# Kernel optimization log

Measured on AMD Instinct MI355X. Metric: run time of the kernel, lower is better.

## Reference

```python
import jax, jax.numpy as jnp
import numpy as np

N = 100000   # nodes
E = 1600000  # edges
IN = 41      # in_channels (21 atom + 20 residue)
ED = 8       # edge_dim
H = 64       # hidden_dim
L = 3        # num_layers
G = 256      # graphs in batch
ATOM = 21
EPS = 1e-5   # GraphNorm eps


def setup_inputs() -> dict:
    key = jax.random.key(0)
    ks = jax.random.split(key, 32)
    s = 0.1
    x = jax.random.normal(ks[0], (N, IN), jnp.float32)
    # make even-index nodes 'ligand' atoms (zero residue part) so both MLP branches fire
    lig = (jnp.arange(N) % 2) == 0
    x = x.at[:, ATOM:].set(jnp.where(lig[:, None], 0.0, x[:, ATOM:]))
    edge_index = jax.random.randint(ks[1], (2, E), 0, N)
    edge_attr = jax.random.normal(ks[2], (E, ED), jnp.float32)
    batch = jnp.sort(jax.random.randint(ks[3], (N,), 0, G))
    p = {
        "lig_W1": s * jax.random.normal(ks[4], (IN, H), jnp.float32),
        "lig_b1": jnp.zeros((H,), jnp.float32),
        "lig_W2": s * jax.random.normal(ks[5], (H, H), jnp.float32),
        "lig_b2": jnp.zeros((H,), jnp.float32),
        "prot_W1": s * jax.random.normal(ks[6], (IN, H), jnp.float32),
        "prot_b1": jnp.zeros((H,), jnp.float32),
        "prot_W2": s * jax.random.normal(ks[7], (H, H), jnp.float32),
        "prot_b2": jnp.zeros((H,), jnp.float32),
        # per-layer stacked params for the 3 GINEConv + GraphNorm blocks
        "conv_We": s * jax.random.normal(ks[8], (L, ED, H), jnp.float32),
        "conv_be": jnp.zeros((L, H), jnp.float32),
        "conv_W1": s * jax.random.normal(ks[9], (L, H, H), jnp.float32),
        "conv_b1": jnp.zeros((L, H), jnp.float32),
        "conv_W2": s * jax.random.normal(ks[10], (L, H, H), jnp.float32),
        "conv_b2": jnp.zeros((L, H), jnp.float32),
        "norm_w": jnp.ones((L, H), jnp.float32),
        "norm_b": jnp.zeros((L, H), jnp.float32),
        "norm_a": jnp.ones((L, H), jnp.float32),  # mean_scale alpha
        "out_W1": s * jax.random.normal(ks[11], (H, H), jnp.float32),
        "out_b1": jnp.zeros((H,), jnp.float32),
        "out_W2": s * jax.random.normal(ks[12], (H, 1), jnp.float32),
        "out_b2": jnp.zeros((1,), jnp.float32),
    }
    return dict(x=x, edge_index=edge_index, edge_attr=edge_attr, batch=batch, **p)


def reference(x, edge_index, edge_attr, batch,
              lig_W1, lig_b1, lig_W2, lig_b2,
              prot_W1, prot_b1, prot_W2, prot_b2,
              conv_We, conv_be, conv_W1, conv_b1, conv_W2, conv_b2,
              norm_w, norm_b, norm_a,
              out_W1, out_b1, out_W2, out_b2):
    # --- input encoder: ligand vs protein branch by residue-part mask ---
    res_mask = jnp.sum(jnp.abs(x[:, ATOM:]), axis=1) > 1e-6
    h_lig = jax.nn.relu(jax.nn.relu(x @ lig_W1 + lig_b1) @ lig_W2 + lig_b2)
    h_prot = jax.nn.relu(jax.nn.relu(x @ prot_W1 + prot_b1) @ prot_W2 + prot_b2)
    h = jnp.where(res_mask[:, None], h_prot, h_lig)  # [N, H]

    src, dst = edge_index[0], edge_index[1]
    counts = jnp.maximum(jax.ops.segment_sum(jnp.ones((N,), h.dtype), batch,
                                             num_segments=G), 1.0)[:, None]  # [G,1]

    for l in range(L):
        # GINEConv (eps=0): nn(h_i + sum_j relu(h_j + lin(e_ij)))
        e = edge_attr @ conv_We[l] + conv_be[l]           # [E, H]
        msg = jax.nn.relu(h[src] + e)                     # [E, H]
        aggr = jax.ops.segment_sum(msg, dst, num_segments=N)
        z = h + aggr
        h = jax.nn.relu(z @ conv_W1[l] + conv_b1[l]) @ conv_W2[l] + conv_b2[l]
        # GraphNorm: (h - alpha*mean_g) / sqrt(var_g + eps) * w + b
        mean = jax.ops.segment_sum(h, batch, num_segments=G) / counts  # [G, H]
        out = h - norm_a[l] * mean[batch]
        var = jax.ops.segment_sum(out * out, batch, num_segments=G) / counts
        h = norm_w[l] * (out / jnp.sqrt(var + EPS)[batch]) + norm_b[l]
        h = jax.nn.relu(h)

    # global_add_pool + readout (dropout = identity at eval)
    g = jax.ops.segment_sum(h, batch, num_segments=G)  # [G, H]
    out = jax.nn.relu(g @ out_W1 + out_b1) @ out_W2 + out_b2  # [G, 1]
    return out.reshape(-1)
```

## Files before the change

### kernel.cpp

```cpp
#include <hip/hip_runtime.h>

#define NN 100000
#define NE 1600000
#define IN_CH 41
#define EDIM 8
#define H 64
#define GNUM 256
#define ATOM 21
#define EPSV 1e-5f
#define EPW 16
#define NTILE (NN / 16)

#define BSH 9
#define NBK 196
#define DPB 512
#define VPT 8
#define EPB (256 * VPT)
#define NBLK_E ((NE + EPB - 1) / EPB)

typedef unsigned short u16;
typedef unsigned int u32;
typedef unsigned long long u64;
typedef __attribute__((ext_vector_type(8))) short short8;
typedef __attribute__((ext_vector_type(4))) float floatx4;

__device__ __forceinline__ u16 f2bf(float f) {
    u32 u = __float_as_uint(f);
    u32 r = (u + 0x7FFFu + ((u >> 16) & 1u)) >> 16;
    return (u16)r;
}
__device__ __forceinline__ float bf2f(u16 u) {
    return __uint_as_float(((u32)u) << 16);
}
__device__ __forceinline__ floatx4 mfma16(short8 a, short8 b, floatx4 c) {
    return __builtin_amdgcn_mfma_f32_16x16x32_bf16(a, b, c, 0, 0, 0);
}
__device__ __forceinline__ short8 pack_bf8(float4 a, float4 b) {
    short8 s;
    s[0] = (short)f2bf(a.x); s[1] = (short)f2bf(a.y);
    s[2] = (short)f2bf(a.z); s[3] = (short)f2bf(a.w);
    s[4] = (short)f2bf(b.x); s[5] = (short)f2bf(b.y);
    s[6] = (short)f2bf(b.z); s[7] = (short)f2bf(b.w);
    return s;
}

__global__ __launch_bounds__(256) void partition_kernel(
    const float* __restrict__ x, int* __restrict__ ctr,
    int* __restrict__ lig_list, int* __restrict__ prot_list)
{
    const int n = blockIdx.x * 256 + threadIdx.x;
    const int lane = threadIdx.x & 63;
    float m = 0.0f;
    if (n < NN) {
        const float* xr = x + (size_t)n * IN_CH + ATOM;
#pragma unroll
        for (int d = 0; d < IN_CH - ATOM; ++d) m += fabsf(xr[d]);
    }
    const bool valid = n < NN;
    const bool prot = valid && (m > 1e-6f);
    const bool lig = valid && !prot;

    const u64 bl = __ballot(lig);
    const u64 bp = __ballot(prot);
    const u64 below_m = (lane == 63) ? (~0ull >> 1) : ((1ull << lane) - 1ull);
    int base_l = 0, base_p = 0;
    if (lane == 0) {
        if (bl) base_l = atomicAdd(&ctr[0], (int)__popcll(bl));
        if (bp) base_p = atomicAdd(&ctr[1], (int)__popcll(bp));
    }
    base_l = __shfl(base_l, 0, 64);
    base_p = __shfl(base_p, 0, 64);
    if (lig)  lig_list [base_l + (int)__popcll(bl & below_m)] = n;
    if (prot) prot_list[base_p + (int)__popcll(bp & below_m)] = n;
}

__global__ __launch_bounds__(256) void xb_kernel(
    const float* __restrict__ x, u16* __restrict__ xb)
{
    const int id = blockIdx.x * 256 + threadIdx.x;
    if (id >= NN * H) return;
    const int n = id >> 6, d = id & 63;
    xb[id] = (d < IN_CH) ? f2bf(x[(size_t)n * IN_CH + d]) : (u16)0;
}

__global__ __launch_bounds__(256) void prep_w_kernel(
    const float* __restrict__ ligW1, const float* __restrict__ ligW2,
    const float* __restrict__ protW1, const float* __restrict__ protW2,
    const float* __restrict__ convW1, const float* __restrict__ convW2,
    u16* __restrict__ wf)
{
    const int id = blockIdx.x * 256 + threadIdx.x;
    if (id >= 10 * 4096) return;
    const int j = id & 7, l = (id >> 3) & 63, t = (id >> 9) & 3;
    const int c = (id >> 11) & 1, mat = id >> 12;
    const int k = c * 32 + ((l >> 4) * 8) + j;
    const int n = t * 16 + (l & 15);
    const float* src; int K = 64;
    if (mat == 0)      { src = ligW1;  K = IN_CH; }
    else if (mat == 1) { src = ligW2; }
    else if (mat == 2) { src = protW1; K = IN_CH; }
    else if (mat == 3) { src = protW2; }
    else {
        const int layer = (mat - 4) >> 1;
        src = (((mat - 4) & 1) ? convW2 : convW1) + (size_t)layer * H * H;
    }
    wf[id] = (k < K) ? f2bf(src[(size_t)k * H + n]) : (u16)0;
}

__global__ __launch_bounds__(256) void enc_mfma_kernel(
    const int* __restrict__ list, const int* __restrict__ countPtr,
    const u16* __restrict__ xb,
    const u16* __restrict__ w1f, const u16* __restrict__ w2f,
    const float* __restrict__ bia1, const float* __restrict__ bia2,
    float* __restrict__ h, u16* __restrict__ h16)
{
    __shared__ __align__(16) u16 hid[4][16 * 72];
    const int wv = threadIdx.x >> 6;
    const int lane = threadIdx.x & 63;
    const int tile = blockIdx.x * 4 + wv;
    const int count = *countPtr;
    if (tile * 16 >= count) return;
    const int quad = lane >> 4;
    const int mi = lane & 15;
    int idx = tile * 16 + mi;
    if (idx >= count) idx = count - 1;
    const int nid = list[idx];

    const short8 a0 = *(const short8*)(xb + (size_t)nid * H + quad * 8);
    const short8 a1 = *(const short8*)(xb + (size_t)nid * H + 32 + quad * 8);

    floatx4 acc[4];
#pragma unroll
    for (int t = 0; t < 4; ++t) acc[t] = (floatx4){0.f, 0.f, 0.f, 0.f};
#pragma unroll
    for (int t = 0; t < 4; ++t) {
        const short8 b0 = *(const short8*)(w1f + ((size_t)(0 * 4 + t) * 64 + lane) * 8);
        const short8 b1 = *(const short8*)(w1f + ((size_t)(1 * 4 + t) * 64 + lane) * 8);
        acc[t] = mfma16(a0, b0, acc[t]);
        acc[t] = mfma16(a1, b1, acc[t]);
    }

    u16* myh = hid[wv];
#pragma unroll
    for (int t = 0; t < 4; ++t) {
        const float bv = bia1[t * 16 + mi];
#pragma unroll
        for (int r = 0; r < 4; ++r) {
            const float v = fmaxf(acc[t][r] + bv, 0.0f);
            myh[(quad * 4 + r) * 72 + t * 16 + mi] = f2bf(v);
        }
    }
    asm volatile("s_waitcnt lgkmcnt(0)" ::: "memory");

    const short8 c0 = *(const short8*)(myh + mi * 72 + quad * 8);
    const short8 c1 = *(const short8*)(myh + mi * 72 + 32 + quad * 8);

    floatx4 acc2[4];
#pragma unroll
    for (int t = 0; t < 4; ++t) acc2[t] = (floatx4){0.f, 0.f, 0.f, 0.f};
#pragma unroll
    for (int t = 0; t < 4; ++t) {
        const short8 b0 = *(const short8*)(w2f + ((size_t)(0 * 4 + t) * 64 + lane) * 8);
        const short8 b1 = *(const short8*)(w2f + ((size_t)(1 * 4 + t) * 64 + lane) * 8);
        acc2[t] = mfma16(c0, b0, acc2[t]);
        acc2[t] = mfma16(c1, b1, acc2[t]);
    }

#pragma unroll
    for (int t = 0; t < 4; ++t) {
        const float bv = bia2[t * 16 + mi];
#pragma unroll
        for (int r = 0; r < 4; ++r) {
            const int row = quad * 4 + r;
            const int nr = __shfl(nid, row, 64);
            if (tile * 16 + row < count) {
                const float v = fmaxf(acc2[t][r] + bv, 0.0f);
                h[(size_t)nr * H + t * 16 + mi] = v;
                h16[(size_t)nr * H + t * 16 + mi] = f2bf(v);
            }
        }
    }
}

__global__ __launch_bounds__(256) void mlp_mfma_kernel(
    const u16* __restrict__ w1f, const u16* __restrict__ w2f,
    const float* __restrict__ bia1, const float* __restrict__ bia2,
    float* __restrict__ h)
{
    __shared__ __align__(16) u16 hid[4][16 * 72];
    const int wv = threadIdx.x >> 6;
    const int lane = threadIdx.x & 63;
    const int tile = blockIdx.x * 4 + wv;
    if (tile >= NTILE) return;
    const int quad = lane >> 4;
    const int mi = lane & 15;
    const int row = tile * 16 + mi;
    const float* zr = h + (size_t)row * H;

    const float4 f0 = *(const float4*)(zr + quad * 8);
    const float4 f1 = *(const float4*)(zr + quad * 8 + 4);
    const float4 f2 = *(const float4*)(zr + 32 + quad * 8);
    const float4 f3 = *(const float4*)(zr + 32 + quad * 8 + 4);
    const short8 a0 = pack_bf8(f0, f1);
    const short8 a1 = pack_bf8(f2, f3);

    floatx4 acc[4];
#pragma unroll
    for (int t = 0; t < 4; ++t) acc[t] = (floatx4){0.f, 0.f, 0.f, 0.f};
#pragma unroll
    for (int t = 0; t < 4; ++t) {
        const short8 b0 = *(const short8*)(w1f + ((size_t)(0 * 4 + t) * 64 + lane) * 8);
        const short8 b1 = *(const short8*)(w1f + ((size_t)(1 * 4 + t) * 64 + lane) * 8);
        acc[t] = mfma16(a0, b0, acc[t]);
        acc[t] = mfma16(a1, b1, acc[t]);
    }

    u16* myh = hid[wv];
#pragma unroll
    for (int t = 0; t < 4; ++t) {
        const float bv = bia1[t * 16 + mi];
#pragma unroll
        for (int r = 0; r < 4; ++r) {
            const float v = fmaxf(acc[t][r] + bv, 0.0f);
            myh[(quad * 4 + r) * 72 + t * 16 + mi] = f2bf(v);
        }
    }
    asm volatile("s_waitcnt lgkmcnt(0)" ::: "memory");

    const short8 c0 = *(const short8*)(myh + mi * 72 + quad * 8);
    const short8 c1 = *(const short8*)(myh + mi * 72 + 32 + quad * 8);

    floatx4 acc2[4];
#pragma unroll
    for (int t = 0; t < 4; ++t) acc2[t] = (floatx4){0.f, 0.f, 0.f, 0.f};
#pragma unroll
    for (int t = 0; t < 4; ++t) {
        const short8 b0 = *(const short8*)(w2f + ((size_t)(0 * 4 + t) * 64 + lane) * 8);
        const short8 b1 = *(const short8*)(w2f + ((size_t)(1 * 4 + t) * 64 + lane) * 8);
        acc2[t] = mfma16(c0, b0, acc2[t]);
        acc2[t] = mfma16(c1, b1, acc2[t]);
    }

#pragma unroll
    for (int t = 0; t < 4; ++t) {
        const float bv = bia2[t * 16 + mi];
#pragma unroll
        for (int r = 0; r < 4; ++r) {
            const int orow = tile * 16 + quad * 4 + r;
            h[(size_t)orow * H + t * 16 + mi] = acc2[t][r] + bv;
        }
    }
}

__global__ void bounds_kernel(const int* __restrict__ batch, int* __restrict__ start)
{
    int g = blockIdx.x * blockDim.x + threadIdx.x;
    if (g > GNUM) return;
    int lo = 0, hi = NN;
    while (lo < hi) {
        int mid = (lo + hi) >> 1;
        if (batch[mid] < g) lo = mid + 1; else hi = mid;
    }
    start[g] = lo;
}

__global__ __launch_bounds__(256) void bhist_kernel(
    const int* __restrict__ ei, int* __restrict__ gbcount)
{
    __shared__ int cnt[NBK];
    const int t = threadIdx.x;
    if (t < NBK) cnt[t] = 0;
    __syncthreads();
    const int base = blockIdx.x * EPB;
#pragma unroll
    for (int v = 0; v < VPT; ++v) {
        const int e = base + v * 256 + t;
        if (e < NE) atomicAdd(&cnt[ei[NE + e] >> BSH], 1);
    }
    __syncthreads();
    if (t < NBK && cnt[t]) atomicAdd(&gbcount[t], cnt[t]);
}

__global__ __launch_bounds__(256) void bscan_kernel(
    const int* __restrict__ gbcount, int* __restrict__ gstart, int* __restrict__ gcur)
{
    __shared__ int s[256];
    const int t = threadIdx.x;
    int v = (t < NBK) ? gbcount[t] : 0;
    s[t] = v;
    __syncthreads();
#pragma unroll
    for (int off = 1; off < 256; off <<= 1) {
        int tmp = (t >= off) ? s[t - off] : 0;
        __syncthreads();
        s[t] += tmp;
        __syncthreads();
    }
    if (t < NBK) { gstart[t] = s[t] - v; gcur[t] = s[t] - v; }
    if (t == 0) gstart[NBK] = NE;
}

__global__ __launch_bounds__(256) void p1_kernel(
    const int* __restrict__ ei, const float* __restrict__ ea,
    int* __restrict__ gcur,
    int2* __restrict__ tmp_sd, uint4* __restrict__ tmp_eab)
{
    __shared__ int cnt[NBK];
    __shared__ int cur[NBK];
    const int t = threadIdx.x;
    if (t < NBK) cnt[t] = 0;
    __syncthreads();
    const int base = blockIdx.x * EPB;
    int dstv[VPT];
#pragma unroll
    for (int v = 0; v < VPT; ++v) {
        const int e = base + v * 256 + t;
        dstv[v] = -1;
        if (e < NE) {
            dstv[v] = ei[NE + e];
            atomicAdd(&cnt[dstv[v] >> BSH], 1);
        }
    }
    __syncthreads();
    if (t < NBK) cur[t] = cnt[t] ? atomicAdd(&gcur[t], cnt[t]) : 0;
    __syncthreads();
#pragma unroll
    for (int v = 0; v < VPT; ++v) {
        const int e = base + v * 256 + t;
        if (e < NE) {
            const int b = dstv[v] >> BSH;
            const int pos = atomicAdd(&cur[b], 1);
            tmp_sd[pos] = make_int2(ei[e], dstv[v]);
            const float4* e4 = (const float4*)(ea + (size_t)e * EDIM);
            float4 a = e4[0], bb = e4[1];
            uint4 u;
            u.x = (u32)f2bf(a.x) | ((u32)f2bf(a.y) << 16);
            u.y = (u32)f2bf(a.z) | ((u32)f2bf(a.w) << 16);
            u.z = (u32)f2bf(bb.x) | ((u32)f2bf(bb.y) << 16);
            u.w = (u32)f2bf(bb.z) | ((u32)f2bf(bb.w) << 16);
            tmp_eab[pos] = u;
        }
    }
}

__global__ __launch_bounds__(1024) void sort_kernel(
    const int2* __restrict__ tmp_sd, const uint4* __restrict__ tmp_eab,
    const int* __restrict__ gstart,
    int2* __restrict__ perm2, uint4* __restrict__ eab)
{
    __shared__ int hist[DPB];
    __shared__ int cursor[DPB];
    const int b = blockIdx.x;
    const int t = threadIdx.x;
    const int s = gstart[b], e = gstart[b + 1];
    const int dbase = b << BSH;

    if (t < DPB) hist[t] = 0;
    __syncthreads();
    for (int i = s + t; i < e; i += 1024)
        atomicAdd(&hist[tmp_sd[i].y - dbase], 1);
    __syncthreads();
    if (t < DPB) cursor[t] = hist[t];
    __syncthreads();
#pragma unroll
    for (int off = 1; off < DPB; off <<= 1) {
        int v = (t < DPB && t >= off) ? cursor[t - off] : 0;
        __syncthreads();
        if (t < DPB) cursor[t] += v;
        __syncthreads();
    }
    if (t < DPB) cursor[t] = s + cursor[t] - hist[t];
    __syncthreads();
    for (int i = s + t; i < e; i += 1024) {
        const int2 sd = tmp_sd[i];
        const int pos = atomicAdd(&cursor[sd.y - dbase], 1);
        perm2[pos] = sd;
        eab[pos] = tmp_eab[i];
    }
}

__global__ __launch_bounds__(256) void aggr_kernel(
    const int2* __restrict__ perm2,
    const u32* __restrict__ eab32,
    const float* __restrict__ We, const float* __restrict__ be,
    const u16* __restrict__ h16, float* __restrict__ h)
{
    const int lane = threadIdx.x & 63;
    const int chunk = blockIdx.x * 4 + (threadIdx.x >> 6);
    const int base = chunk * EPW;

    float we_r[EDIM];
#pragma unroll
    for (int d = 0; d < EDIM; ++d) we_r[d] = We[d * H + lane];
    const float be_r = be[lane];

    const int2 pd = perm2[base + (lane & 15)];
    const u32 eu = eab32[(size_t)base * 4 + lane];

    float hv[EPW];
#pragma unroll
    for (int j = 0; j < EPW; ++j) {
        const int sj = __builtin_amdgcn_readlane(pd.x, j);
        hv[j] = bf2f(h16[(size_t)sj * H + lane]);
    }

    float acc = 0.0f;
    int cur = __builtin_amdgcn_readlane(pd.y, 0);
#pragma unroll
    for (int j = 0; j < EPW; ++j) {
        const int dj = __builtin_amdgcn_readlane(pd.y, j);
        float msg = be_r;
#pragma unroll
        for (int p = 0; p < 4; ++p) {
            const u32 w2 = __builtin_amdgcn_readlane(eu, j * 4 + p);
            msg = fmaf(__uint_as_float(w2 << 16), we_r[2 * p], msg);
            msg = fmaf(__uint_as_float(w2 & 0xffff0000u), we_r[2 * p + 1], msg);
        }
        if (dj != cur) {
            unsafeAtomicAdd(&h[(size_t)cur * H + lane], acc);
            acc = 0.0f;
            cur = dj;
        }
        acc += fmaxf(hv[j] + msg, 0.0f);
    }
    unsafeAtomicAdd(&h[(size_t)cur * H + lane], acc);
}

__global__ __launch_bounds__(1024) void graphnorm_kernel(
    float* __restrict__ h, u16* __restrict__ h16,
    const int* __restrict__ start,
    const float* __restrict__ w, const float* __restrict__ b,
    const float* __restrict__ a,
    float* __restrict__ pool, int do_pool)
{
    __shared__ float red1[16][H], red2[16][H];
    __shared__ float amean_s[H], rstd_s[H];
    const int g = blockIdx.x;
    const int lane = threadIdx.x & 63;
    const int wv = threadIdx.x >> 6;
    const int s = start[g], e = start[g + 1];

    float s1 = 0.f, s2 = 0.f;
    for (int i = s + wv; i < e; i += 16) {
        float v = h[(size_t)i * H + lane];
        s1 += v; s2 += v * v;
    }
    red1[wv][lane] = s1; red2[wv][lane] = s2;
    __syncthreads();
    if (threadIdx.x < H) {
        float t1 = 0.f, t2 = 0.f;
#pragma unroll
        for (int k = 0; k < 16; ++k) { t1 += red1[k][lane]; t2 += red2[k][lane]; }
        float cnt = fmaxf((float)(e - s), 1.0f);
        float mean = t1 / cnt;
        float alpha = a[lane];
        float var = t2 / cnt - (2.0f * alpha - alpha * alpha) * mean * mean;
        var = fmaxf(var, 0.0f);
        amean_s[lane] = alpha * mean;
        rstd_s[lane] = rsqrtf(var + EPSV);
    }
    __syncthreads();
    const float am = amean_s[lane], rstd = rstd_s[lane];
    const float ww = w[lane], bb = b[lane];
    float ps = 0.f;
    for (int i = s + wv; i < e; i += 16) {
        float v = (h[(size_t)i * H + lane] - am) * rstd * ww + bb;
        v = fmaxf(v, 0.0f);
        h[(size_t)i * H + lane] = v;
        h16[(size_t)i * H + lane] = f2bf(v);
        ps += v;
    }
    if (do_pool && e > s) unsafeAtomicAdd(&pool[g * H + lane], ps);
}

__global__ __launch_bounds__(64) void final_kernel(
    const float* __restrict__ pool,
    const float* __restrict__ W1, const float* __restrict__ b1,
    const float* __restrict__ W2, const float* __restrict__ b2,
    float* __restrict__ out)
{
    const int g = blockIdx.x;
    const int lane = threadIdx.x;
    const float gv = pool[g * H + lane];
    float acc = b1[lane];
#pragma unroll
    for (int d = 0; d < H; ++d)
        acc = fmaf(__shfl(gv, d, 64), W1[d * H + lane], acc);
    float r = fmaxf(acc, 0.0f);
    float v = r * W2[lane];
#pragma unroll
    for (int o = 32; o > 0; o >>= 1) v += __shfl_xor(v, o, 64);
    if (lane == 0) out[g] = v + b2[0];
}

extern "C" void kernel_launch(void* const* d_in, const int* in_sizes, int n_in,
                              void* d_out, int out_size, void* d_ws, size_t ws_size,
                              hipStream_t stream)
{
    const float* x      = (const float*)d_in[0];
    const int*   ei     = (const int*)  d_in[1];
    const float* ea     = (const float*)d_in[2];
    const int*   batch  = (const int*)  d_in[3];
    const float* ligW1  = (const float*)d_in[4];
    const float* ligb1  = (const float*)d_in[5];
    const float* ligW2  = (const float*)d_in[6];
    const float* ligb2  = (const float*)d_in[7];
    const float* protW1 = (const float*)d_in[8];
    const float* protb1 = (const float*)d_in[9];
    const float* protW2 = (const float*)d_in[10];
    const float* protb2 = (const float*)d_in[11];
    const float* convWe = (const float*)d_in[12];
    const float* convbe = (const float*)d_in[13];
    const float* convW1 = (const float*)d_in[14];
    const float* convb1 = (const float*)d_in[15];
    const float* convW2 = (const float*)d_in[16];
    const float* convb2 = (const float*)d_in[17];
    const float* normw  = (const float*)d_in[18];
    const float* normb  = (const float*)d_in[19];
    const float* norma  = (const float*)d_in[20];
    const float* outW1  = (const float*)d_in[21];
    const float* outb1  = (const float*)d_in[22];
    const float* outW2  = (const float*)d_in[23];
    const float* outb2  = (const float*)d_in[24];

    float* out = (float*)d_out;

    float* h         = (float*)d_ws;
    uint4* eab       = (uint4*)(h + (size_t)NN * H);
    int2*  perm2     = (int2*)(eab + (size_t)NE);
    u16*   h16       = (u16*)(perm2 + (size_t)NE);
    u16*   xb        = h16 + (size_t)NN * H;
    u16*   wf        = xb + (size_t)NN * H;
    uint4* tmp_eab   = (uint4*)h;
    int2*  tmp_sd    = (int2*)h16;

    int*   ctr       = (int*)(wf + 40960);
    int*   gbcount   = ctr + 2;
    float* pool      = (float*)(gbcount + NBK);
    int*   gstart    = (int*)(pool + GNUM * H);
    int*   gcur      = gstart + (NBK + 1);
    int*   start     = gcur + NBK;
    int*   lig_list  = start + (GNUM + 1);
    int*   prot_list = lig_list + NN;

    hipMemsetAsync(ctr, 0, ((size_t)2 + NBK + GNUM * H) * sizeof(int), stream);

    xb_kernel<<<(NN * H + 255) / 256, 256, 0, stream>>>(x, xb);
    prep_w_kernel<<<(10 * 4096 + 255) / 256, 256, 0, stream>>>(
        ligW1, ligW2, protW1, protW2, convW1, convW2, wf);
    partition_kernel<<<(NN + 255) / 256, 256, 0, stream>>>(x, ctr, lig_list, prot_list);
    bounds_kernel<<<2, 256, 0, stream>>>(batch, start);

    bhist_kernel<<<NBLK_E, 256, 0, stream>>>(ei, gbcount);
    bscan_kernel<<<1, 256, 0, stream>>>(gbcount, gstart, gcur);
    p1_kernel<<<NBLK_E, 256, 0, stream>>>(ei, ea, gcur, tmp_sd, tmp_eab);
    sort_kernel<<<NBK, 1024, 0, stream>>>(tmp_sd, tmp_eab, gstart, perm2, eab);

    const int enc_blocks = (NTILE + 3) / 4;
    enc_mfma_kernel<<<enc_blocks, 256, 0, stream>>>(
        lig_list, &ctr[0], xb, wf + 0 * 4096, wf + 1 * 4096, ligb1, ligb2, h, h16);
    enc_mfma_kernel<<<enc_blocks, 256, 0, stream>>>(
        prot_list, &ctr[1], xb, wf + 2 * 4096, wf + 3 * 4096, protb1, protb2, h, h16);

    const int aggr_blocks = NE / EPW / 4;
    const int mlp_blocks = (NTILE + 3) / 4;
    for (int l = 0; l < 3; ++l) {
        aggr_kernel<<<aggr_blocks, 256, 0, stream>>>(
            perm2, (const u32*)eab,
            convWe + (size_t)l * EDIM * H, convbe + (size_t)l * H, h16, h);
        mlp_mfma_kernel<<<mlp_blocks, 256, 0, stream>>>(
            wf + (size_t)(4 + 2 * l) * 4096, wf + (size_t)(5 + 2 * l) * 4096,
            convb1 + (size_t)l * H, convb2 + (size_t)l * H, h);
        graphnorm_kernel<<<GNUM, 1024, 0, stream>>>(
            h, h16, start, normw + (size_t)l * H, normb + (size_t)l * H,
            norma + (size_t)l * H, pool, (l == 2) ? 1 : 0);
    }
    final_kernel<<<GNUM, 64, 0, stream>>>(pool, outW1, outb1, outW2, outb2, out);
}
```

Baseline: 617.6 us.

## Defer edge-attr bf16 packing to sort pass and enlarge p1 blocks

The first bucketing pass no longer reads and converts edge attributes. It only writes a 16-byte record of (src, dst, original edge id, pad) per edge, using 1024-thread blocks so each block covers more edges and issues fewer global atomics on the bucket cursors. The sort kernel then gathers the fp32 edge attributes by original id, packs them to bf16 and writes them in final order. This removes one staged write and re-read of the packed attributes, but adds a scattered 32-byte gather per edge in the sort pass and a wider temporary record.

```diff
diff --git a/kernel.cpp b/kernel.cpp
--- a/kernel.cpp
+++ b/kernel.cpp
@@ -17,6 +17,8 @@
 #define VPT 8
 #define EPB (256 * VPT)
 #define NBLK_E ((NE + EPB - 1) / EPB)
+#define EPB_P1 (1024 * VPT)
+#define NBLK_P1 ((NE + EPB_P1 - 1) / EPB_P1)
 
 typedef unsigned short u16;
 typedef unsigned int u32;
@@ -300,21 +302,21 @@
     if (t == 0) gstart[NBK] = NE;
 }
 
-__global__ __launch_bounds__(256) void p1_kernel(
-    const int* __restrict__ ei, const float* __restrict__ ea,
+__global__ __launch_bounds__(1024) void p1_kernel(
+    const int* __restrict__ ei,
     int* __restrict__ gcur,
-    int2* __restrict__ tmp_sd, uint4* __restrict__ tmp_eab)
+    int4* __restrict__ tmp_sde)
 {
     __shared__ int cnt[NBK];
     __shared__ int cur[NBK];
     const int t = threadIdx.x;
     if (t < NBK) cnt[t] = 0;
     __syncthreads();
-    const int base = blockIdx.x * EPB;
+    const int base = blockIdx.x * EPB_P1;
     int dstv[VPT];
 #pragma unroll
     for (int v = 0; v < VPT; ++v) {
-        const int e = base + v * 256 + t;
+        const int e = base + v * 1024 + t;
         dstv[v] = -1;
         if (e < NE) {
             dstv[v] = ei[NE + e];
@@ -326,25 +328,17 @@
     __syncthreads();
 #pragma unroll
     for (int v = 0; v < VPT; ++v) {
-        const int e = base + v * 256 + t;
+        const int e = base + v * 1024 + t;
         if (e < NE) {
             const int b = dstv[v] >> BSH;
             const int pos = atomicAdd(&cur[b], 1);
-            tmp_sd[pos] = make_int2(ei[e], dstv[v]);
-            const float4* e4 = (const float4*)(ea + (size_t)e * EDIM);
-            float4 a = e4[0], bb = e4[1];
-            uint4 u;
-            u.x = (u32)f2bf(a.x) | ((u32)f2bf(a.y) << 16);
-            u.y = (u32)f2bf(a.z) | ((u32)f2bf(a.w) << 16);
-            u.z = (u32)f2bf(bb.x) | ((u32)f2bf(bb.y) << 16);
-            u.w = (u32)f2bf(bb.z) | ((u32)f2bf(bb.w) << 16);
-            tmp_eab[pos] = u;
+            tmp_sde[pos] = make_int4(ei[e], dstv[v], e, 0);
         }
     }
 }
 
 __global__ __launch_bounds__(1024) void sort_kernel(
-    const int2* __restrict__ tmp_sd, const uint4* __restrict__ tmp_eab,
+    const int4* __restrict__ tmp_sde, const float* __restrict__ ea,
     const int* __restrict__ gstart,
     int2* __restrict__ perm2, uint4* __restrict__ eab)
 {
@@ -358,7 +352,7 @@
     if (t < DPB) hist[t] = 0;
     __syncthreads();
     for (int i = s + t; i < e; i += 1024)
-        atomicAdd(&hist[tmp_sd[i].y - dbase], 1);
+        atomicAdd(&hist[tmp_sde[i].y - dbase], 1);
     __syncthreads();
     if (t < DPB) cursor[t] = hist[t];
     __syncthreads();
@@ -372,10 +366,17 @@
     if (t < DPB) cursor[t] = s + cursor[t] - hist[t];
     __syncthreads();
     for (int i = s + t; i < e; i += 1024) {
-        const int2 sd = tmp_sd[i];
-        const int pos = atomicAdd(&cursor[sd.y - dbase], 1);
-        perm2[pos] = sd;
-        eab[pos] = tmp_eab[i];
+        const int4 sde = tmp_sde[i];
+        const float4* e4 = (const float4*)(ea + (size_t)sde.z * EDIM);
+        const float4 a = e4[0], bb = e4[1];
+        uint4 u;
+        u.x = (u32)f2bf(a.x) | ((u32)f2bf(a.y) << 16);
+        u.y = (u32)f2bf(a.z) | ((u32)f2bf(a.w) << 16);
+        u.z = (u32)f2bf(bb.x) | ((u32)f2bf(bb.y) << 16);
+        u.w = (u32)f2bf(bb.z) | ((u32)f2bf(bb.w) << 16);
+        const int pos = atomicAdd(&cursor[sde.y - dbase], 1);
+        perm2[pos] = make_int2(sde.x, sde.y);
+        eab[pos] = u;
     }
 }
 
@@ -531,8 +532,7 @@
     u16*   h16       = (u16*)(perm2 + (size_t)NE);
     u16*   xb        = h16 + (size_t)NN * H;
     u16*   wf        = xb + (size_t)NN * H;
-    uint4* tmp_eab   = (uint4*)h;
-    int2*  tmp_sd    = (int2*)h16;
+    int4*  tmp_sde   = (int4*)h;
 
     int*   ctr       = (int*)(wf + 40960);
     int*   gbcount   = ctr + 2;
@@ -553,8 +553,8 @@
 
     bhist_kernel<<<NBLK_E, 256, 0, stream>>>(ei, gbcount);
     bscan_kernel<<<1, 256, 0, stream>>>(gbcount, gstart, gcur);
-    p1_kernel<<<NBLK_E, 256, 0, stream>>>(ei, ea, gcur, tmp_sd, tmp_eab);
-    sort_kernel<<<NBK, 1024, 0, stream>>>(tmp_sd, tmp_eab, gstart, perm2, eab);
+    p1_kernel<<<NBLK_P1, 1024, 0, stream>>>(ei, gcur, tmp_sde);
+    sort_kernel<<<NBK, 1024, 0, stream>>>(tmp_sde, ea, gstart, perm2, eab);
 
     const int enc_blocks = (NTILE + 3) / 4;
     enc_mfma_kernel<<<enc_blocks, 256, 0, stream>>>(
```

After: 614.6 us. About the same (-0.5%).
